# Kernel tuning notes

Hardware: AMD Instinct MI355X
Metric: run time of the kernel (lower is better)

Reference implementation:

```python
import jax, jax.numpy as jnp
import numpy as np

N_TOTAL = 2_000_000
F_DIM = 128
NUM_GRAPHS = 16384


def setup_inputs() -> dict:
    key = jax.random.key(0)
    k1, k2, k3, k4 = jax.random.split(key, 4)
    x = jax.random.normal(k1, (N_TOTAL, F_DIM), dtype=jnp.float32)
    batch_idx = jnp.sort(jax.random.randint(k2, (N_TOTAL,), 0, NUM_GRAPHS, dtype=jnp.int32))
    # nn.Linear(in_dim, 1): weight [1, in_dim], bias [1]
    bound = 1.0 / np.sqrt(F_DIM)
    attn_w = jax.random.uniform(k3, (F_DIM,), dtype=jnp.float32, minval=-bound, maxval=bound)
    attn_b = jax.random.uniform(k4, (), dtype=jnp.float32, minval=-bound, maxval=bound)
    return {"x": x, "attn_w": attn_w, "attn_b": attn_b, "batch_idx": batch_idx, "num_graphs": NUM_GRAPHS}


def reference(x, attn_w, attn_b, batch_idx, num_graphs):
    # logits = Linear(x).squeeze(-1): [N]
    logits = x @ attn_w + attn_b
    # segment softmax over nodes grouped by graph id (pyg_softmax)
    seg_max = jax.ops.segment_max(logits, batch_idx, num_segments=num_graphs)  # [G]
    # guard empty segments (-inf) so gather stays finite
    seg_max = jnp.where(jnp.isfinite(seg_max), seg_max, 0.0)
    shifted = logits - seg_max[batch_idx]
    expv = jnp.exp(shifted)
    seg_sum = jax.ops.segment_sum(expv, batch_idx, num_segments=num_graphs)  # [G]
    alpha = expv / (seg_sum[batch_idx] + 1e-16)  # [N]
    # weighted scatter-add: [G, F]
    pooled = jax.ops.segment_sum(x * alpha[:, None], batch_idx, num_segments=num_graphs)
    return pooled
```

## Files before the change

### kernel.cpp

```cpp
#include <hip/hip_runtime.h>
#include <math.h>

#define F_DIM 128
#define CHUNK 2048

__global__ __launch_bounds__(256)
void node_attn_pool_kernel(const float* __restrict__ x,
                           const float* __restrict__ attn_w,
                           const int*   __restrict__ bidx,
                           float* __restrict__ out,
                           int n_total) {
    const int g    = blockIdx.x;
    const int tid  = threadIdx.x;
    const int lane = tid & 63;
    const int wave = tid >> 6;

    int lo = 0, hi = n_total;
    while (lo < hi) { int mid = (lo + hi) >> 1; if (bidx[mid] < g)     lo = mid + 1; else hi = mid; }
    const int start = lo;
    hi = n_total;
    while (lo < hi) { int mid = (lo + hi) >> 1; if (bidx[mid] < g + 1) lo = mid + 1; else hi = mid; }
    const int end = lo;

    __shared__ float lds_e[CHUNK];
    __shared__ float red[4];
    __shared__ float s_bcast;
    __shared__ float accbuf[F_DIM];

    const float2 w2 = ((const float2*)attn_w)[lane];

    const int r = tid >> 7;
    const int f = tid & 127;

    float m_run = -INFINITY;
    float l_run = 0.f;
    float acc   = 0.f;

    for (int s = start; s < end; s += CHUNK) {
        const int c = min(CHUNK, end - s);

        for (int j = wave; j < c; j += 4) {
            const float2 xv = ((const float2*)(x + (size_t)(s + j) * F_DIM))[lane];
            float d = xv.x * w2.x + xv.y * w2.y;
            #pragma unroll
            for (int off = 32; off > 0; off >>= 1) d += __shfl_down(d, off);
            if (lane == 0) lds_e[j] = d;
        }
        __syncthreads();

        float cm = -INFINITY;
        for (int j = tid; j < c; j += 256) cm = fmaxf(cm, lds_e[j]);
        #pragma unroll
        for (int off = 32; off > 0; off >>= 1) cm = fmaxf(cm, __shfl_down(cm, off));
        if (lane == 0) red[wave] = cm;
        __syncthreads();
        if (tid == 0) s_bcast = fmaxf(fmaxf(red[0], red[1]), fmaxf(red[2], red[3]));
        __syncthreads();

        const float m_new = fmaxf(m_run, s_bcast);
        const float scale = __expf(m_run - m_new);
        l_run *= scale;
        acc   *= scale;
        m_run  = m_new;

        float csum = 0.f;
        for (int j = tid; j < c; j += 256) {
            const float e = __expf(lds_e[j] - m_new);
            lds_e[j] = e;
            csum += e;
        }
        #pragma unroll
        for (int off = 32; off > 0; off >>= 1) csum += __shfl_down(csum, off);
        if (lane == 0) red[wave] = csum;
        __syncthreads();
        l_run += red[0] + red[1] + red[2] + red[3];

        for (int j = r; j < c; j += 2) {
            acc += lds_e[j] * x[(size_t)(s + j) * F_DIM + f];
        }
        __syncthreads();
    }

    if (r == 1) accbuf[f] = acc;
    __syncthreads();
    if (r == 0) {
        const float tot = acc + accbuf[f];
        out[(size_t)g * F_DIM + f] = tot / (l_run + 1e-16f);
    }
}

extern "C" void kernel_launch(void* const* d_in, const int* in_sizes, int n_in,
                              void* d_out, int out_size, void* d_ws, size_t ws_size,
                              hipStream_t stream) {
    const float* x      = (const float*)d_in[0];
    const float* attn_w = (const float*)d_in[1];
    const int*   bidx   = (const int*)d_in[3];

    const int n_total    = in_sizes[0] / F_DIM;
    const int num_graphs = out_size / F_DIM;

    node_attn_pool_kernel<<<num_graphs, 256, 0, stream>>>(
        x, attn_w, bidx, (float*)d_out, n_total);
}
```

Before: 1.549 ms.

## Precompute segment bounds and hold node chunk in registers for single x read

Adds a separate kernel that computes segment start offsets from the sorted batch index, replacing the per-block binary searches. The main kernel now loads each 64-node chunk of x once as float4 into registers, computes logits with half-wave shuffles, and reuses those registers for the weighted accumulation instead of reading x a second time. The aim is to halve global traffic on x and widen the loads, at the cost of an extra launch and more barriers per small chunk. With about 122 nodes per graph, each block handles roughly two chunks.

```diff
diff --git a/kernel.cpp b/kernel.cpp
--- a/kernel.cpp
+++ b/kernel.cpp
@@ -2,90 +2,131 @@
 #include <math.h>
 
 #define F_DIM 128
-#define CHUNK 2048
+#define CHUNK 64
+
+__global__ void seg_bounds_kernel(const int* __restrict__ bidx,
+                                  int* __restrict__ seg, int n, int G) {
+    int i = blockIdx.x * blockDim.x + threadIdx.x;
+    if (i >= n) return;
+    int cur = bidx[i];
+    if (i == 0) {
+        for (int g = 0; g <= cur; ++g) seg[g] = 0;
+    } else {
+        int prev = bidx[i - 1];
+        for (int g = prev + 1; g <= cur; ++g) seg[g] = i;
+    }
+    if (i == n - 1) {
+        for (int g = cur + 1; g <= G; ++g) seg[g] = n;
+    }
+}
 
 __global__ __launch_bounds__(256)
 void node_attn_pool_kernel(const float* __restrict__ x,
                            const float* __restrict__ attn_w,
-                           const int*   __restrict__ bidx,
-                           float* __restrict__ out,
-                           int n_total) {
+                           const int*   __restrict__ seg,
+                           float* __restrict__ out) {
     const int g    = blockIdx.x;
     const int tid  = threadIdx.x;
     const int lane = tid & 63;
     const int wave = tid >> 6;
+    const int grp  = tid >> 5;
+    const int fq   = tid & 31;
 
-    int lo = 0, hi = n_total;
-    while (lo < hi) { int mid = (lo + hi) >> 1; if (bidx[mid] < g)     lo = mid + 1; else hi = mid; }
-    const int start = lo;
-    hi = n_total;
-    while (lo < hi) { int mid = (lo + hi) >> 1; if (bidx[mid] < g + 1) lo = mid + 1; else hi = mid; }
-    const int end = lo;
+    const int start = seg[g];
+    const int end   = seg[g + 1];
 
+    __shared__ float lds_logit[CHUNK];
     __shared__ float lds_e[CHUNK];
-    __shared__ float red[4];
-    __shared__ float s_bcast;
-    __shared__ float accbuf[F_DIM];
+    __shared__ float s_m, s_l;
+    __shared__ float lds_red[4 * F_DIM];
 
-    const float2 w2 = ((const float2*)attn_w)[lane];
-
-    const int r = tid >> 7;
-    const int f = tid & 127;
+    const float4 w4 = ((const float4*)attn_w)[fq];
 
     float m_run = -INFINITY;
     float l_run = 0.f;
-    float acc   = 0.f;
+    float4 acc  = make_float4(0.f, 0.f, 0.f, 0.f);
+    float4 x4[8];
+
+    const float4* xp = (const float4*)x;
 
     for (int s = start; s < end; s += CHUNK) {
         const int c = min(CHUNK, end - s);
+        const size_t cbase = (size_t)s * (F_DIM / 4);
 
-        for (int j = wave; j < c; j += 4) {
-            const float2 xv = ((const float2*)(x + (size_t)(s + j) * F_DIM))[lane];
-            float d = xv.x * w2.x + xv.y * w2.y;
-            #pragma unroll
-            for (int off = 32; off > 0; off >>= 1) d += __shfl_down(d, off);
-            if (lane == 0) lds_e[j] = d;
+        #pragma unroll
+        for (int i = 0; i < 8; ++i) {
+            const int ri = i * 8 + grp;
+            float4 v = make_float4(0.f, 0.f, 0.f, 0.f);
+            if (ri < c) v = xp[cbase + (size_t)i * 256 + tid];
+            x4[i] = v;
+            float d = v.x * w4.x + v.y * w4.y + v.z * w4.z + v.w * w4.w;
+            d += __shfl_down(d, 16, 32);
+            d += __shfl_down(d,  8, 32);
+            d += __shfl_down(d,  4, 32);
+            d += __shfl_down(d,  2, 32);
+            d += __shfl_down(d,  1, 32);
+            if (fq == 0 && ri < c) lds_logit[ri] = d;
         }
         __syncthreads();
 
-        float cm = -INFINITY;
-        for (int j = tid; j < c; j += 256) cm = fmaxf(cm, lds_e[j]);
-        #pragma unroll
-        for (int off = 32; off > 0; off >>= 1) cm = fmaxf(cm, __shfl_down(cm, off));
-        if (lane == 0) red[wave] = cm;
-        __syncthreads();
-        if (tid == 0) s_bcast = fmaxf(fmaxf(red[0], red[1]), fmaxf(red[2], red[3]));
+        if (wave == 0) {
+            float v = (lane < c) ? lds_logit[lane] : -INFINITY;
+            v = fmaxf(v, __shfl_down(v, 32));
+            v = fmaxf(v, __shfl_down(v, 16));
+            v = fmaxf(v, __shfl_down(v,  8));
+            v = fmaxf(v, __shfl_down(v,  4));
+            v = fmaxf(v, __shfl_down(v,  2));
+            v = fmaxf(v, __shfl_down(v,  1));
+            if (lane == 0) s_m = v;
+        }
         __syncthreads();
 
-        const float m_new = fmaxf(m_run, s_bcast);
+        const float m_new = fmaxf(m_run, s_m);
         const float scale = __expf(m_run - m_new);
+        m_run  = m_new;
         l_run *= scale;
-        acc   *= scale;
-        m_run  = m_new;
+        acc.x *= scale; acc.y *= scale; acc.z *= scale; acc.w *= scale;
 
-        float csum = 0.f;
-        for (int j = tid; j < c; j += 256) {
-            const float e = __expf(lds_e[j] - m_new);
-            lds_e[j] = e;
-            csum += e;
+        if (wave == 0) {
+            float e = (lane < c) ? __expf(lds_logit[lane] - m_new) : 0.f;
+            if (lane < c) lds_e[lane] = e;
+            e += __shfl_down(e, 32);
+            e += __shfl_down(e, 16);
+            e += __shfl_down(e,  8);
+            e += __shfl_down(e,  4);
+            e += __shfl_down(e,  2);
+            e += __shfl_down(e,  1);
+            if (lane == 0) s_l = e;
         }
+        __syncthreads();
+
+        l_run += s_l;
+
         #pragma unroll
-        for (int off = 32; off > 0; off >>= 1) csum += __shfl_down(csum, off);
-        if (lane == 0) red[wave] = csum;
-        __syncthreads();
-        l_run += red[0] + red[1] + red[2] + red[3];
-
-        for (int j = r; j < c; j += 2) {
-            acc += lds_e[j] * x[(size_t)(s + j) * F_DIM + f];
+        for (int i = 0; i < 8; ++i) {
+            const int ri = i * 8 + grp;
+            if (ri < c) {
+                const float e = lds_e[ri];
+                acc.x += e * x4[i].x;
+                acc.y += e * x4[i].y;
+                acc.z += e * x4[i].z;
+                acc.w += e * x4[i].w;
+            }
         }
         __syncthreads();
     }
 
-    if (r == 1) accbuf[f] = acc;
+    acc.x += __shfl_down(acc.x, 32);
+    acc.y += __shfl_down(acc.y, 32);
+    acc.z += __shfl_down(acc.z, 32);
+    acc.w += __shfl_down(acc.w, 32);
+    if (lane < 32) ((float4*)(lds_red + wave * F_DIM))[lane] = acc;
     __syncthreads();
-    if (r == 0) {
-        const float tot = acc + accbuf[f];
-        out[(size_t)g * F_DIM + f] = tot / (l_run + 1e-16f);
+
+    if (tid < F_DIM) {
+        const float tot = lds_red[tid] + lds_red[F_DIM + tid] +
+                          lds_red[2 * F_DIM + tid] + lds_red[3 * F_DIM + tid];
+        out[(size_t)g * F_DIM + tid] = tot / (l_run + 1e-16f);
     }
 }
 
@@ -99,6 +140,11 @@
     const int n_total    = in_sizes[0] / F_DIM;
     const int num_graphs = out_size / F_DIM;
 
+    int* seg = (int*)d_ws;
+
+    seg_bounds_kernel<<<(n_total + 255) / 256, 256, 0, stream>>>(
+        bidx, seg, n_total, num_graphs);
+
     node_attn_pool_kernel<<<num_graphs, 256, 0, stream>>>(
-        x, attn_w, bidx, (float*)d_out, n_total);
+        x, attn_w, seg, (float*)d_out);
 }
```

Result: faster. 1.286 ms (-17.0%).
